# Performance work log

Measured on AMD Instinct MI355X. Metric: run time of the kernel, lower is better.

Reference implementation:

```python
import jax, jax.numpy as jnp
import numpy as np

B, S = 1, 2048
HID, INTER = 4096, 11008
HEADS, HD = 32, 128
GS = 128
EPS = 1e-6
BASE = 10000.0
IMIN, IMAX = -(2**31), 2**31 - 1


def _rope_tables():
    inv_freq = 1.0 / (BASE ** (np.arange(0, HD, 2, dtype=np.float32) / HD))
    t = np.arange(S, dtype=np.float32)
    freqs = np.outer(t, inv_freq)            # [S, HD/2]
    emb = np.concatenate([freqs, freqs], -1)  # [S, HD]
    return jnp.asarray(np.sin(emb), jnp.float32), jnp.asarray(np.cos(emb), jnp.float32)


def setup_inputs() -> dict:
    key = jax.random.key(0)
    ks = iter(jax.random.split(key, 40))
    def qset(in_f, out_f):
        qw = jax.random.randint(next(ks), (in_f // 8, out_f), IMIN, IMAX, dtype=jnp.int32)
        qz = jax.random.randint(next(ks), (in_f // GS, out_f // 8), IMIN, IMAX, dtype=jnp.int32)
        sc = jax.random.uniform(next(ks), (in_f // GS, out_f), dtype=jnp.float32) * 0.01 + 1e-3
        return qw, qz, sc
    dims = {"q": (HID, HID), "k": (HID, HID), "v": (HID, HID), "o": (HID, HID),
            "gate": (HID, INTER), "up": (HID, INTER), "down": (INTER, HID)}
    inp = {}
    for name, (i, o) in dims.items():
        qw, qz, sc = qset(i, o)
        inp["qw_" + name] = qw
        inp["qz_" + name] = qz
        inp["sc_" + name] = sc
    inp["hidden_states"] = jax.random.normal(next(ks), (B, S, HID), dtype=jnp.float32)
    inp["ln1_w"] = jnp.ones((HID,), jnp.float32)
    inp["ln2_w"] = jnp.ones((HID,), jnp.float32)
    sin, cos = _rope_tables()
    inp["sin"] = sin
    inp["cos"] = cos
    # causal additive mask, as stored in ExLlamaBuffer.attn_mask (past_len = 0)
    mask = jnp.where(jnp.tril(jnp.ones((S, S), bool)), 0.0, -1e9).astype(jnp.float32)
    inp["attn_mask"] = mask[None, None]
    return inp


def _dequant(qw, qz, sc):
    # GPTQ int4: qweight [in/8, out] packs 8 rows per int32; qzeros [groups, out/8]
    in_f, out_f = qw.shape[0] * 8, qw.shape[1]
    groups = sc.shape[0]
    sh = jnp.arange(8, dtype=jnp.int32) * 4
    w = ((qw[:, None, :] >> sh[None, :, None]) & 15)
    w = w.reshape(groups, in_f // groups, out_f).astype(jnp.float32)
    z = ((qz[:, :, None] >> sh[None, None, :]) & 15).reshape(groups, out_f).astype(jnp.float32)
    return ((w - (z + 1.0)[:, None, :]) * sc[:, None, :]).reshape(in_f, out_f)


def _rms(x, w):
    v = jnp.mean(x * x, axis=-1, keepdims=True)
    return x * jax.lax.rsqrt(v + EPS) * w


def _rot_half(x):
    x1, x2 = jnp.split(x, 2, axis=-1)
    return jnp.concatenate([-x2, x1], axis=-1)


def reference(qw_q, qz_q, sc_q, qw_k, qz_k, sc_k, qw_v, qz_v, sc_v,
              qw_o, qz_o, sc_o, qw_gate, qz_gate, sc_gate,
              qw_up, qz_up, sc_up, qw_down, qz_down, sc_down,
              hidden_states, ln1_w, ln2_w, sin, cos, attn_mask):
    lin = lambda x, a, b, c: x @ _dequant(a, b, c)
    h = hidden_states
    # attention block
    x = _rms(h, ln1_w)
    q = lin(x, qw_q, qz_q, sc_q).reshape(B, S, HEADS, HD).transpose(0, 2, 1, 3)
    k = lin(x, qw_k, qz_k, sc_k).reshape(B, S, HEADS, HD).transpose(0, 2, 1, 3)
    v = lin(x, qw_v, qz_v, sc_v).reshape(B, S, HEADS, HD).transpose(0, 2, 1, 3)
    c, s = cos[None, None], sin[None, None]  # [1,1,S,HD]
    q = q * c + _rot_half(q) * s
    k = k * c + _rot_half(k) * s
    scores = jnp.einsum('bhqd,bhkd->bhqk', q, k) / np.float32(np.sqrt(HD)) + attn_mask
    p = jax.nn.softmax(scores, axis=-1)
    o = jnp.einsum('bhqk,bhkd->bhqd', p, v).transpose(0, 2, 1, 3).reshape(B, S, HID)
    h = h + lin(o, qw_o, qz_o, sc_o)
    # MLP block
    x = _rms(h, ln2_w)
    y = jax.nn.silu(lin(x, qw_gate, qz_gate, sc_gate)) * lin(x, qw_up, qz_up, sc_up)
    return h + lin(y, qw_down, qz_down, sc_down)
```

## Files before the change

kernel.cpp:

```cpp
#include <hip/hip_runtime.h>
#include <cstdint>
#include <cstddef>

#define S_LEN 2048
#define HID   4096
#define INTER 11008
#define NHEADS 32
#define HD    128

typedef __attribute__((ext_vector_type(4))) float  f32x4;
typedef __attribute__((ext_vector_type(8))) __bf16 bf16x8;
typedef __attribute__((ext_vector_type(8))) short  s16x8;
typedef __attribute__((ext_vector_type(4))) short  s16x4;

__device__ __forceinline__ float bf2f(short s) {
  unsigned u = ((unsigned)(unsigned short)s) << 16;
  return __builtin_bit_cast(float, u);
}
__device__ __forceinline__ short f2bf(float f) {
  unsigned u = __builtin_bit_cast(unsigned, f);
  u += 0x7FFFu + ((u >> 16) & 1u);
  return (short)(u >> 16);
}
__device__ __forceinline__ f32x4 mfma16(s16x8 a, s16x8 b, f32x4 c) {
  return __builtin_amdgcn_mfma_f32_16x16x32_bf16(
      __builtin_bit_cast(bf16x8, a), __builtin_bit_cast(bf16x8, b), c, 0, 0, 0);
}
__device__ __forceinline__ void gload_lds16(const void* g, void* l) {
  __builtin_amdgcn_global_load_lds(
      (const __attribute__((address_space(1))) void*)g,
      (__attribute__((address_space(3))) void*)l, 16, 0, 0);
}

__global__ __launch_bounds__(256) void rmsnorm_kernel(const float* __restrict__ x,
                                                      const float* __restrict__ w,
                                                      short* __restrict__ out) {
  int row = blockIdx.x;
  const float* xr = x + (size_t)row * HID;
  short* orow = out + (size_t)row * HID;
  int tid = threadIdx.x;
  f32x4 v[4];
  float ss = 0.f;
#pragma unroll
  for (int i = 0; i < 4; ++i) {
    v[i] = ((const f32x4*)xr)[i * 256 + tid];
    ss += v[i][0] * v[i][0] + v[i][1] * v[i][1] + v[i][2] * v[i][2] + v[i][3] * v[i][3];
  }
#pragma unroll
  for (int off = 32; off > 0; off >>= 1) ss += __shfl_xor(ss, off);
  __shared__ float psum[4];
  if ((tid & 63) == 0) psum[tid >> 6] = ss;
  __syncthreads();
  float tot = psum[0] + psum[1] + psum[2] + psum[3];
  float r = rsqrtf(tot * (1.0f / (float)HID) + 1e-6f);
#pragma unroll
  for (int i = 0; i < 4; ++i) {
    int base = (i * 256 + tid) * 4;
    s16x4 o;
#pragma unroll
    for (int j = 0; j < 4; ++j) o[j] = f2bf(v[i][j] * r * w[base + j]);
    *(s16x4*)&orow[base] = o;
  }
}

__global__ __launch_bounds__(256) void dequant_kernel(const int* __restrict__ qw,
                                                      const int* __restrict__ qz,
                                                      const float* __restrict__ sc,
                                                      short* __restrict__ wt,
                                                      int N, int noff, int Kext) {
  __shared__ short tile[64 * 72];
  int n0 = blockIdx.x * 64;
  int k0 = blockIdx.y * 64;
  int g = k0 >> 7;
  int qr0 = k0 >> 3;
  int t = threadIdx.x;
#pragma unroll
  for (int i = 0; i < 2; ++i) {
    int idx = t + i * 256;
    int r = idx >> 6;
    int n = idx & 63;
    int gc = noff + n0 + n;
    unsigned q = (unsigned)qw[(size_t)(qr0 + r) * N + gc];
    float s = sc[(size_t)g * N + gc];
    unsigned zq = (unsigned)qz[(size_t)g * (N >> 3) + (gc >> 3)];
    float zs = ((float)((zq >> ((gc & 7) * 4)) & 15u) + 1.0f) * s;
    s16x8 o;
#pragma unroll
    for (int j = 0; j < 8; ++j)
      o[j] = f2bf(fmaf((float)((q >> (4 * j)) & 15u), s, -zs));
    *(s16x8*)&tile[n * 72 + r * 8] = o;
  }
  __syncthreads();
  int n = t >> 2;
#pragma unroll
  for (int i = 0; i < 2; ++i) {
    int c = (t & 3) + i * 4;
    *(s16x8*)&wt[(size_t)(n0 + n) * Kext + k0 + c * 8] = *(const s16x8*)&tile[n * 72 + c * 8];
  }
}

template <int OMODE>
__global__ __launch_bounds__(256) void gemm_kernel(const short* __restrict__ A, int lda,
                                                   const short* __restrict__ BT, int ldb,
                                                   void* __restrict__ Cv, int ldc,
                                                   const float* __restrict__ base,
                                                   int Kext) {
  __shared__ short As[2][128 * 32];
  __shared__ short Bs[2][128 * 32];
  int nwg = gridDim.x * gridDim.y;
  int lid = blockIdx.y * gridDim.x + blockIdx.x;
  int cpx = nwg >> 3;
  int swz = (lid & 7) * cpx + (lid >> 3);
  int bn = swz % gridDim.x, bm = swz / gridDim.x;
  int tid = threadIdx.x;
  int lane = tid & 63, wv = tid >> 6;
  int wr = wv >> 1, wc = wv & 1;
  f32x4 acc[4][4] = {};
  int nk = Kext >> 5;
  int lr = lane >> 2;
  int lc = lane & 3;
  const short* Abase = A + (size_t)(bm * 128) * lda;
  const short* Bbase = BT + (size_t)(bn * 128) * ldb;

  auto stage = [&](int buf, int t) {
    int k0 = t << 5;
#pragma unroll
    for (int i = 0; i < 2; ++i) {
      int r = i * 64 + wv * 16 + lr;
      gload_lds16(Abase + (size_t)r * lda + k0 + lc * 8, &As[buf][i * 2048 + wv * 512]);
      gload_lds16(Bbase + (size_t)r * ldb + k0 + lc * 8, &Bs[buf][i * 2048 + wv * 512]);
    }
  };
  auto compute = [&](int buf) {
    int kc = (lane >> 4) * 8;
    int ra = wr * 64 + (lane & 15);
    int rb = wc * 64 + (lane & 15);
    s16x8 af[4], bfr[4];
#pragma unroll
    for (int m = 0; m < 4; ++m) af[m] = *(const s16x8*)&As[buf][(ra + m * 16) * 32 + kc];
#pragma unroll
    for (int n = 0; n < 4; ++n) bfr[n] = *(const s16x8*)&Bs[buf][(rb + n * 16) * 32 + kc];
#pragma unroll
    for (int m = 0; m < 4; ++m)
#pragma unroll
      for (int n = 0; n < 4; ++n) acc[m][n] = mfma16(af[m], bfr[n], acc[m][n]);
  };

  stage(0, 0);
  __syncthreads();
  for (int t = 0; t < nk; ++t) {
    if (t + 1 < nk) stage((t + 1) & 1, t + 1);
    compute(t & 1);
    __syncthreads();
  }

  int row0 = bm * 128 + wr * 64 + ((lane >> 4) << 2);
  int col0 = bn * 128 + wc * 64 + (lane & 15);
#pragma unroll
  for (int m = 0; m < 4; ++m)
#pragma unroll
    for (int n = 0; n < 4; ++n)
#pragma unroll
      for (int j = 0; j < 4; ++j) {
        size_t idx = (size_t)(row0 + m * 16 + j) * ldc + col0 + n * 16;
        if (OMODE == 0)      ((short*)Cv)[idx] = f2bf(acc[m][n][j]);
        else if (OMODE == 1) ((float*)Cv)[idx] = base[idx] + acc[m][n][j];
        else                 ((float*)Cv)[idx] = ((float*)Cv)[idx] + acc[m][n][j];
      }
}

__global__ __launch_bounds__(128) void rope_kernel(short* __restrict__ q, short* __restrict__ k,
                                                   const float* __restrict__ sp,
                                                   const float* __restrict__ cp) {
  int s = blockIdx.x, h = blockIdx.y;
  short* p = (blockIdx.z ? k : q) + (size_t)s * HID + h * HD;
  int d = threadIdx.x;
  float x = bf2f(p[d]);
  float xp = bf2f(p[d ^ 64]);
  float rot = (d < 64) ? -xp : xp;
  float y = x * cp[s * HD + d] + rot * sp[s * HD + d];
  __syncthreads();
  p[d] = f2bf(y);
}

__global__ __launch_bounds__(256, 2) void attn_kernel(const short* __restrict__ qb,
                                                      const short* __restrict__ kb,
                                                      const short* __restrict__ vb,
                                                      short* __restrict__ ob) {
  int qt = (int)(gridDim.x - 1) - blockIdx.x;
  int h = blockIdx.y;
  int tid = threadIdx.x, lane = tid & 63, wv = tid >> 6;
  __shared__ short Kl[64 * 128];
  __shared__ short Vl[128 * 72];
  __shared__ short Pl[4][32 * 72];
  int q0 = qt * 128 + wv * 32;
  s16x8 qf[2][4];
#pragma unroll
  for (int m = 0; m < 2; ++m)
#pragma unroll
    for (int kf = 0; kf < 4; ++kf) {
      int r = q0 + m * 16 + (lane & 15);
      int d = kf * 32 + (lane >> 4) * 8;
      qf[m][kf] = *(const s16x8*)&qb[(size_t)r * HID + h * HD + d];
    }
  f32x4 o[2][8] = {};
  float mrow[2][4], lrow[2][4];
#pragma unroll
  for (int m = 0; m < 2; ++m)
#pragma unroll
    for (int j = 0; j < 4; ++j) { mrow[m][j] = -1e30f; lrow[m][j] = 0.f; }

  auto load_tile = [&](int kv0, s16x8* kr, s16x8* vr) {
#pragma unroll
    for (int i = 0; i < 4; ++i) {
      int cid = tid + i * 256;
      int kv = cid >> 4, c = cid & 15;
      kr[i] = *(const s16x8*)(kb + (size_t)(kv0 + kv) * HID + h * HD + c * 8);
      vr[i] = *(const s16x8*)(vb + (size_t)(kv0 + kv) * HID + h * HD + c * 8);
    }
  };
  auto store_tile = [&](const s16x8* kr, const s16x8* vr) {
#pragma unroll
    for (int i = 0; i < 4; ++i) {
      int cid = tid + i * 256;
      int kv = cid >> 4, c = cid & 15;
      *(s16x8*)((char*)Kl + kv * 256 + ((c ^ (kv & 7)) * 16)) = kr[i];
      int kvs = kv ^ ((c & 7) << 3);
#pragma unroll
      for (int j = 0; j < 8; ++j) Vl[(c * 8 + j) * 72 + kvs] = vr[i][j];
    }
  };

  const float scale = 0.08838834764831845f;
  int kv_end = qt * 128 + 128;
  s16x8 kra[4], vra[4], krb[4], vrb[4];
  load_tile(0, kra, vra);
  store_tile(kra, vra);
  __syncthreads();
  for (int kv0 = 0; kv0 < kv_end; kv0 += 64) {
    bool more = kv0 + 64 < kv_end;
    if (more) load_tile(kv0 + 64, krb, vrb);

    f32x4 sfr[2][4] = {};
    __builtin_amdgcn_s_setprio(1);
#pragma unroll
    for (int nf = 0; nf < 4; ++nf) {
      s16x8 kfr[4];
      int kvr = nf * 16 + (lane & 15);
#pragma unroll
      for (int kf = 0; kf < 4; ++kf) {
        int cc = (kf * 4 + (lane >> 4)) ^ (kvr & 7);
        kfr[kf] = *(const s16x8*)((const char*)Kl + kvr * 256 + cc * 16);
      }
#pragma unroll
      for (int m = 0; m < 2; ++m)
#pragma unroll
        for (int kf = 0; kf < 4; ++kf) sfr[m][nf] = mfma16(qf[m][kf], kfr[kf], sfr[m][nf]);
    }
    __builtin_amdgcn_s_setprio(0);
#pragma unroll
    for (int m = 0; m < 2; ++m)
#pragma unroll
      for (int j = 0; j < 4; ++j) {
        int qrow = q0 + m * 16 + (lane >> 4) * 4 + j;
        float pm = -1e30f;
#pragma unroll
        for (int nf = 0; nf < 4; ++nf) {
          int kvc = kv0 + nf * 16 + (lane & 15);
          float v = sfr[m][nf][j] * scale;
          v = (kvc <= qrow) ? v : -1e30f;
          sfr[m][nf][j] = v;
          pm = fmaxf(pm, v);
        }
#pragma unroll
        for (int off = 1; off < 16; off <<= 1) pm = fmaxf(pm, __shfl_xor(pm, off));
        float mnew = fmaxf(mrow[m][j], pm);
        float alpha = __expf(mrow[m][j] - mnew);
        mrow[m][j] = mnew;
        float rs = 0.f;
#pragma unroll
        for (int nf = 0; nf < 4; ++nf) {
          float p = __expf(sfr[m][nf][j] - mnew);
          sfr[m][nf][j] = p;
          rs += p;
        }
#pragma unroll
        for (int off = 1; off < 16; off <<= 1) rs += __shfl_xor(rs, off);
        lrow[m][j] = lrow[m][j] * alpha + rs;
#pragma unroll
        for (int nd = 0; nd < 8; ++nd) o[m][nd][j] *= alpha;
      }
#pragma unroll
    for (int m = 0; m < 2; ++m)
#pragma unroll
      for (int nf = 0; nf < 4; ++nf)
#pragma unroll
        for (int j = 0; j < 4; ++j)
          Pl[wv][(m * 16 + (lane >> 4) * 4 + j) * 72 + nf * 16 + (lane & 15)] =
              f2bf(sfr[m][nf][j]);
    s16x8 pa[2][2];
#pragma unroll
    for (int m = 0; m < 2; ++m)
#pragma unroll
      for (int kf = 0; kf < 2; ++kf)
        pa[m][kf] = *(const s16x8*)&Pl[wv][(m * 16 + (lane & 15)) * 72 + kf * 32 + (lane >> 4) * 8];
    __builtin_amdgcn_s_setprio(1);
#pragma unroll
    for (int nd = 0; nd < 8; ++nd) {
      s16x8 vf[2];
      int drow = nd * 16 + (lane & 15);
      int key = ((drow >> 3) & 7) << 3;
#pragma unroll
      for (int kf = 0; kf < 2; ++kf)
        vf[kf] = *(const s16x8*)&Vl[drow * 72 + ((kf * 32 + (lane >> 4) * 8) ^ key)];
#pragma unroll
      for (int m = 0; m < 2; ++m)
#pragma unroll
        for (int kf = 0; kf < 2; ++kf) o[m][nd] = mfma16(pa[m][kf], vf[kf], o[m][nd]);
    }
    __builtin_amdgcn_s_setprio(0);
    __syncthreads();
    if (more) store_tile(krb, vrb);
    __syncthreads();
  }
#pragma unroll
  for (int m = 0; m < 2; ++m)
#pragma unroll
    for (int nd = 0; nd < 8; ++nd)
#pragma unroll
      for (int j = 0; j < 4; ++j) {
        int r = q0 + m * 16 + (lane >> 4) * 4 + j;
        int c = h * HD + nd * 16 + (lane & 15);
        ob[(size_t)r * HID + c] = f2bf(o[m][nd][j] / lrow[m][j]);
      }
}

__global__ __launch_bounds__(256) void silumul_kernel(const short* __restrict__ g,
                                                      const short* __restrict__ u,
                                                      short* __restrict__ y) {
  size_t idx = (size_t)blockIdx.x * 256 + threadIdx.x;
  s16x8 gv = ((const s16x8*)g)[idx];
  s16x8 uv = ((const s16x8*)u)[idx];
  s16x8 yv;
#pragma unroll
  for (int j = 0; j < 8; ++j) {
    float gf = bf2f(gv[j]);
    float uf = bf2f(uv[j]);
    float sl = gf / (1.f + __expf(-gf));
    yv[j] = f2bf(sl * uf);
  }
  ((s16x8*)y)[idx] = yv;
}

extern "C" void kernel_launch(void* const* d_in, const int* in_sizes, int n_in,
                              void* d_out, int out_size, void* d_ws, size_t ws_size,
                              hipStream_t stream) {
  const int* qw[7]; const int* qz[7]; const float* sc[7];
  for (int i = 0; i < 7; ++i) {
    qw[i] = (const int*)d_in[i * 3 + 0];
    qz[i] = (const int*)d_in[i * 3 + 1];
    sc[i] = (const float*)d_in[i * 3 + 2];
  }
  const float* hin  = (const float*)d_in[21];
  const float* ln1  = (const float*)d_in[22];
  const float* ln2  = (const float*)d_in[23];
  const float* sinp = (const float*)d_in[24];
  const float* cosp = (const float*)d_in[25];
  float* out = (float*)d_out;

  char* ws = (char*)d_ws;
  const size_t MB = 1024 * 1024;
  short* XB    = (short*)(ws);
  short* WDQ   = (short*)(ws + 16 * MB);
  short* QB    = (short*)(ws + 48 * MB);
  short* KB    = (short*)(ws + 64 * MB);
  short* VB    = (short*)(ws + 80 * MB);
  short* OB    = (short*)(ws + 96 * MB);
  short* GATEB = (short*)(ws + 48 * MB);
  short* UPB   = (short*)(ws + 91 * MB);

  dim3 blk(256);
  dim3 dq44(64, 64);
  dim3 gm_hid(HID / 128, S_LEN / 128);

  rmsnorm_kernel<<<S_LEN, blk, 0, stream>>>(hin, ln1, XB);
  short* qkv_out[3] = {QB, KB, VB};
  for (int i = 0; i < 3; ++i) {
    dequant_kernel<<<dq44, blk, 0, stream>>>(qw[i], qz[i], sc[i], WDQ, HID, 0, HID);
    gemm_kernel<0><<<gm_hid, blk, 0, stream>>>(XB, HID, WDQ, HID, qkv_out[i], HID, nullptr, HID);
  }
  rope_kernel<<<dim3(S_LEN, NHEADS, 2), dim3(128), 0, stream>>>(QB, KB, sinp, cosp);
  attn_kernel<<<dim3(S_LEN / 128, NHEADS), blk, 0, stream>>>(QB, KB, VB, OB);
  dequant_kernel<<<dq44, blk, 0, stream>>>(qw[3], qz[3], sc[3], WDQ, HID, 0, HID);
  gemm_kernel<1><<<gm_hid, blk, 0, stream>>>(OB, HID, WDQ, HID, out, HID, hin, HID);
  rmsnorm_kernel<<<S_LEN, blk, 0, stream>>>(out, ln2, XB);
  const int noffs[3] = {0, 4096, 8192};
  const int nexts[3] = {4096, 4096, 2816};
  for (int c = 0; c < 3; ++c) {
    dequant_kernel<<<dim3(nexts[c] / 64, 64), blk, 0, stream>>>(qw[4], qz[4], sc[4], WDQ, INTER, noffs[c], HID);
    gemm_kernel<0><<<dim3(nexts[c] / 128, 16), blk, 0, stream>>>(XB, HID, WDQ, HID, GATEB + noffs[c], INTER, nullptr, HID);
  }
  for (int c = 0; c < 3; ++c) {
    dequant_kernel<<<dim3(nexts[c] / 64, 64), blk, 0, stream>>>(qw[5], qz[5], sc[5], WDQ, INTER, noffs[c], HID);
    gemm_kernel<0><<<dim3(nexts[c] / 128, 16), blk, 0, stream>>>(XB, HID, WDQ, HID, UPB + noffs[c], INTER, nullptr, HID);
  }
  silumul_kernel<<<(S_LEN * (size_t)INTER) / 8 / 256, blk, 0, stream>>>(GATEB, UPB, GATEB);
  for (int c = 0; c < 3; ++c) {
    int koff = noffs[c], kx = nexts[c];
    dequant_kernel<<<dim3(64, kx / 64), blk, 0, stream>>>(
        qw[6] + (size_t)(koff >> 3) * HID, qz[6] + (size_t)(koff >> 7) * (HID / 8),
        sc[6] + (size_t)(koff >> 7) * HID, WDQ, HID, 0, kx);
    gemm_kernel<2><<<gm_hid, blk, 0, stream>>>(GATEB + koff, INTER, WDQ, kx, out, HID, nullptr, kx);
  }
}
```

Baseline: 1.582 ms.

## Overlap next weight dequant with current GEMM in a combined kernel launch

Merges dequant and GEMM into one kernel whose grid splits into GEMM blocks and dequant blocks. Each launch runs a GEMM on one ping-pong weight buffer while dequantizing the next weight into the other buffer, which removes serialization between dequant and GEMM launches. The SiLU-multiply is fused into the up-projection epilogue, dropping the separate elementwise pass and the UP buffer. Attention launch bounds change to one block per SM, and Q is staged in the output buffer. Buffer aliasing and chunk offsets are intricate, so a small indexing error could corrupt results.

```diff
diff --git a/kernel.cpp b/kernel.cpp
--- a/kernel.cpp
+++ b/kernel.cpp
@@ -63,110 +63,115 @@
   }
 }
 
-__global__ __launch_bounds__(256) void dequant_kernel(const int* __restrict__ qw,
-                                                      const int* __restrict__ qz,
-                                                      const float* __restrict__ sc,
-                                                      short* __restrict__ wt,
-                                                      int N, int noff, int Kext) {
-  __shared__ short tile[64 * 72];
-  int n0 = blockIdx.x * 64;
-  int k0 = blockIdx.y * 64;
-  int g = k0 >> 7;
-  int qr0 = k0 >> 3;
-  int t = threadIdx.x;
-#pragma unroll
-  for (int i = 0; i < 2; ++i) {
-    int idx = t + i * 256;
-    int r = idx >> 6;
-    int n = idx & 63;
-    int gc = noff + n0 + n;
-    unsigned q = (unsigned)qw[(size_t)(qr0 + r) * N + gc];
-    float s = sc[(size_t)g * N + gc];
-    unsigned zq = (unsigned)qz[(size_t)g * (N >> 3) + (gc >> 3)];
-    float zs = ((float)((zq >> ((gc & 7) * 4)) & 15u) + 1.0f) * s;
-    s16x8 o;
-#pragma unroll
-    for (int j = 0; j < 8; ++j)
-      o[j] = f2bf(fmaf((float)((q >> (4 * j)) & 15u), s, -zs));
-    *(s16x8*)&tile[n * 72 + r * 8] = o;
+template <int OMODE>
+__global__ __launch_bounds__(256) void paired_kernel(
+    const short* __restrict__ A, int lda,
+    const short* __restrict__ BT, int ldb,
+    void* __restrict__ Cv, int ldc,
+    const float* __restrict__ base, int Kext,
+    int gnx, int gny,
+    const int* __restrict__ qw, const int* __restrict__ qz,
+    const float* __restrict__ sc, short* __restrict__ wt,
+    int N, int noff, int dnx, int dqld) {
+  __shared__ short sm[4 * 4096];
+  int bid = blockIdx.x;
+  int gtot = gnx * gny;
+  int tid = threadIdx.x;
+  if (bid < gtot) {
+    int cpx = gtot >> 3;
+    int swz = (bid & 7) * cpx + (bid >> 3);
+    int bn = swz % gnx, bm = swz / gnx;
+    int lane = tid & 63, wv = tid >> 6;
+    int wr = wv >> 1, wc = wv & 1;
+    f32x4 acc[4][4] = {};
+    int nk = Kext >> 5;
+    int lr = lane >> 2, lc = lane & 3;
+    const short* Abase = A + (size_t)(bm * 128) * lda;
+    const short* Bbase = BT + (size_t)(bn * 128) * ldb;
+    short* As0 = sm;
+    short* Bs0 = sm + 8192;
+
+    auto stage = [&](int buf, int t) {
+      int k0 = t << 5;
+#pragma unroll
+      for (int i = 0; i < 2; ++i) {
+        int r = i * 64 + wv * 16 + lr;
+        gload_lds16(Abase + (size_t)r * lda + k0 + lc * 8, As0 + buf * 4096 + i * 2048 + wv * 512);
+        gload_lds16(Bbase + (size_t)r * ldb + k0 + lc * 8, Bs0 + buf * 4096 + i * 2048 + wv * 512);
+      }
+    };
+    auto compute = [&](int buf) {
+      int kc = (lane >> 4) * 8;
+      int ra = wr * 64 + (lane & 15);
+      int rb = wc * 64 + (lane & 15);
+      s16x8 af[4], bfr[4];
+#pragma unroll
+      for (int m = 0; m < 4; ++m) af[m] = *(const s16x8*)&As0[buf * 4096 + (ra + m * 16) * 32 + kc];
+#pragma unroll
+      for (int n = 0; n < 4; ++n) bfr[n] = *(const s16x8*)&Bs0[buf * 4096 + (rb + n * 16) * 32 + kc];
+#pragma unroll
+      for (int m = 0; m < 4; ++m)
+#pragma unroll
+        for (int n = 0; n < 4; ++n) acc[m][n] = mfma16(af[m], bfr[n], acc[m][n]);
+    };
+
+    stage(0, 0);
+    __syncthreads();
+    for (int t = 0; t < nk; ++t) {
+      if (t + 1 < nk) stage((t + 1) & 1, t + 1);
+      compute(t & 1);
+      __syncthreads();
+    }
+
+    int row0 = bm * 128 + wr * 64 + ((lane >> 4) << 2);
+    int col0 = bn * 128 + wc * 64 + (lane & 15);
+#pragma unroll
+    for (int m = 0; m < 4; ++m)
+#pragma unroll
+      for (int n = 0; n < 4; ++n)
+#pragma unroll
+        for (int j = 0; j < 4; ++j) {
+          size_t idx = (size_t)(row0 + m * 16 + j) * ldc + col0 + n * 16;
+          if (OMODE == 0)      ((short*)Cv)[idx] = f2bf(acc[m][n][j]);
+          else if (OMODE == 1) ((float*)Cv)[idx] = base[idx] + acc[m][n][j];
+          else if (OMODE == 2) ((float*)Cv)[idx] = ((float*)Cv)[idx] + acc[m][n][j];
+          else {
+            short* C = (short*)Cv;
+            float g = bf2f(C[idx]);
+            float sl = g / (1.f + __expf(-g));
+            C[idx] = f2bf(sl * acc[m][n][j]);
+          }
+        }
+  } else {
+    int id = bid - gtot;
+    int n0 = (id % dnx) * 64;
+    int k0 = (id / dnx) * 64;
+    int g = k0 >> 7;
+    int qr0 = k0 >> 3;
+#pragma unroll
+    for (int i = 0; i < 2; ++i) {
+      int idx = tid + i * 256;
+      int r = idx >> 6;
+      int n = idx & 63;
+      int gc = noff + n0 + n;
+      unsigned q = (unsigned)qw[(size_t)(qr0 + r) * N + gc];
+      float s = sc[(size_t)g * N + gc];
+      unsigned zq = (unsigned)qz[(size_t)g * (N >> 3) + (gc >> 3)];
+      float zs = ((float)((zq >> ((gc & 7) * 4)) & 15u) + 1.0f) * s;
+      s16x8 o;
+#pragma unroll
+      for (int j = 0; j < 8; ++j)
+        o[j] = f2bf(fmaf((float)((q >> (4 * j)) & 15u), s, -zs));
+      *(s16x8*)&sm[n * 72 + r * 8] = o;
+    }
+    __syncthreads();
+    int n = tid >> 2;
+#pragma unroll
+    for (int i = 0; i < 2; ++i) {
+      int c = (tid & 3) + i * 4;
+      *(s16x8*)&wt[(size_t)(n0 + n) * dqld + k0 + c * 8] = *(const s16x8*)&sm[n * 72 + c * 8];
+    }
   }
-  __syncthreads();
-  int n = t >> 2;
-#pragma unroll
-  for (int i = 0; i < 2; ++i) {
-    int c = (t & 3) + i * 4;
-    *(s16x8*)&wt[(size_t)(n0 + n) * Kext + k0 + c * 8] = *(const s16x8*)&tile[n * 72 + c * 8];
-  }
-}
-
-template <int OMODE>
-__global__ __launch_bounds__(256) void gemm_kernel(const short* __restrict__ A, int lda,
-                                                   const short* __restrict__ BT, int ldb,
-                                                   void* __restrict__ Cv, int ldc,
-                                                   const float* __restrict__ base,
-                                                   int Kext) {
-  __shared__ short As[2][128 * 32];
-  __shared__ short Bs[2][128 * 32];
-  int nwg = gridDim.x * gridDim.y;
-  int lid = blockIdx.y * gridDim.x + blockIdx.x;
-  int cpx = nwg >> 3;
-  int swz = (lid & 7) * cpx + (lid >> 3);
-  int bn = swz % gridDim.x, bm = swz / gridDim.x;
-  int tid = threadIdx.x;
-  int lane = tid & 63, wv = tid >> 6;
-  int wr = wv >> 1, wc = wv & 1;
-  f32x4 acc[4][4] = {};
-  int nk = Kext >> 5;
-  int lr = lane >> 2;
-  int lc = lane & 3;
-  const short* Abase = A + (size_t)(bm * 128) * lda;
-  const short* Bbase = BT + (size_t)(bn * 128) * ldb;
-
-  auto stage = [&](int buf, int t) {
-    int k0 = t << 5;
-#pragma unroll
-    for (int i = 0; i < 2; ++i) {
-      int r = i * 64 + wv * 16 + lr;
-      gload_lds16(Abase + (size_t)r * lda + k0 + lc * 8, &As[buf][i * 2048 + wv * 512]);
-      gload_lds16(Bbase + (size_t)r * ldb + k0 + lc * 8, &Bs[buf][i * 2048 + wv * 512]);
-    }
-  };
-  auto compute = [&](int buf) {
-    int kc = (lane >> 4) * 8;
-    int ra = wr * 64 + (lane & 15);
-    int rb = wc * 64 + (lane & 15);
-    s16x8 af[4], bfr[4];
-#pragma unroll
-    for (int m = 0; m < 4; ++m) af[m] = *(const s16x8*)&As[buf][(ra + m * 16) * 32 + kc];
-#pragma unroll
-    for (int n = 0; n < 4; ++n) bfr[n] = *(const s16x8*)&Bs[buf][(rb + n * 16) * 32 + kc];
-#pragma unroll
-    for (int m = 0; m < 4; ++m)
-#pragma unroll
-      for (int n = 0; n < 4; ++n) acc[m][n] = mfma16(af[m], bfr[n], acc[m][n]);
-  };
-
-  stage(0, 0);
-  __syncthreads();
-  for (int t = 0; t < nk; ++t) {
-    if (t + 1 < nk) stage((t + 1) & 1, t + 1);
-    compute(t & 1);
-    __syncthreads();
-  }
-
-  int row0 = bm * 128 + wr * 64 + ((lane >> 4) << 2);
-  int col0 = bn * 128 + wc * 64 + (lane & 15);
-#pragma unroll
-  for (int m = 0; m < 4; ++m)
-#pragma unroll
-    for (int n = 0; n < 4; ++n)
-#pragma unroll
-      for (int j = 0; j < 4; ++j) {
-        size_t idx = (size_t)(row0 + m * 16 + j) * ldc + col0 + n * 16;
-        if (OMODE == 0)      ((short*)Cv)[idx] = f2bf(acc[m][n][j]);
-        else if (OMODE == 1) ((float*)Cv)[idx] = base[idx] + acc[m][n][j];
-        else                 ((float*)Cv)[idx] = ((float*)Cv)[idx] + acc[m][n][j];
-      }
 }
 
 __global__ __launch_bounds__(128) void rope_kernel(short* __restrict__ q, short* __restrict__ k,
@@ -183,7 +188,7 @@
   p[d] = f2bf(y);
 }
 
-__global__ __launch_bounds__(256, 2) void attn_kernel(const short* __restrict__ qb,
+__global__ __launch_bounds__(256, 1) void attn_kernel(const short* __restrict__ qb,
                                                       const short* __restrict__ kb,
                                                       const short* __restrict__ vb,
                                                       short* __restrict__ ob) {
@@ -333,23 +338,6 @@
         int c = h * HD + nd * 16 + (lane & 15);
         ob[(size_t)r * HID + c] = f2bf(o[m][nd][j] / lrow[m][j]);
       }
-}
-
-__global__ __launch_bounds__(256) void silumul_kernel(const short* __restrict__ g,
-                                                      const short* __restrict__ u,
-                                                      short* __restrict__ y) {
-  size_t idx = (size_t)blockIdx.x * 256 + threadIdx.x;
-  s16x8 gv = ((const s16x8*)g)[idx];
-  s16x8 uv = ((const s16x8*)u)[idx];
-  s16x8 yv;
-#pragma unroll
-  for (int j = 0; j < 8; ++j) {
-    float gf = bf2f(gv[j]);
-    float uf = bf2f(uv[j]);
-    float sl = gf / (1.f + __expf(-gf));
-    yv[j] = f2bf(sl * uf);
-  }
-  ((s16x8*)y)[idx] = yv;
 }
 
 extern "C" void kernel_launch(void* const* d_in, const int* in_sizes, int n_in,
@@ -371,45 +359,57 @@
   char* ws = (char*)d_ws;
   const size_t MB = 1024 * 1024;
   short* XB    = (short*)(ws);
-  short* WDQ   = (short*)(ws + 16 * MB);
-  short* QB    = (short*)(ws + 48 * MB);
-  short* KB    = (short*)(ws + 64 * MB);
-  short* VB    = (short*)(ws + 80 * MB);
-  short* OB    = (short*)(ws + 96 * MB);
-  short* GATEB = (short*)(ws + 48 * MB);
-  short* UPB   = (short*)(ws + 91 * MB);
+  short* WA    = (short*)(ws + 16 * MB);
+  short* WB    = (short*)(ws + 48 * MB);
+  short* KB    = (short*)(ws + 80 * MB);
+  short* VB    = (short*)(ws + 96 * MB);
+  short* OB    = (short*)(ws + 112 * MB);
+  short* GATEB = (short*)(ws + 80 * MB);
+  short* QBd   = (short*)d_out;
 
   dim3 blk(256);
-  dim3 dq44(64, 64);
-  dim3 gm_hid(HID / 128, S_LEN / 128);
-
-  rmsnorm_kernel<<<S_LEN, blk, 0, stream>>>(hin, ln1, XB);
-  short* qkv_out[3] = {QB, KB, VB};
-  for (int i = 0; i < 3; ++i) {
-    dequant_kernel<<<dq44, blk, 0, stream>>>(qw[i], qz[i], sc[i], WDQ, HID, 0, HID);
-    gemm_kernel<0><<<gm_hid, blk, 0, stream>>>(XB, HID, WDQ, HID, qkv_out[i], HID, nullptr, HID);
-  }
-  rope_kernel<<<dim3(S_LEN, NHEADS, 2), dim3(128), 0, stream>>>(QB, KB, sinp, cosp);
-  attn_kernel<<<dim3(S_LEN / 128, NHEADS), blk, 0, stream>>>(QB, KB, VB, OB);
-  dequant_kernel<<<dq44, blk, 0, stream>>>(qw[3], qz[3], sc[3], WDQ, HID, 0, HID);
-  gemm_kernel<1><<<gm_hid, blk, 0, stream>>>(OB, HID, WDQ, HID, out, HID, hin, HID);
-  rmsnorm_kernel<<<S_LEN, blk, 0, stream>>>(out, ln2, XB);
   const int noffs[3] = {0, 4096, 8192};
   const int nexts[3] = {4096, 4096, 2816};
-  for (int c = 0; c < 3; ++c) {
-    dequant_kernel<<<dim3(nexts[c] / 64, 64), blk, 0, stream>>>(qw[4], qz[4], sc[4], WDQ, INTER, noffs[c], HID);
-    gemm_kernel<0><<<dim3(nexts[c] / 128, 16), blk, 0, stream>>>(XB, HID, WDQ, HID, GATEB + noffs[c], INTER, nullptr, HID);
-  }
-  for (int c = 0; c < 3; ++c) {
-    dequant_kernel<<<dim3(nexts[c] / 64, 64), blk, 0, stream>>>(qw[5], qz[5], sc[5], WDQ, INTER, noffs[c], HID);
-    gemm_kernel<0><<<dim3(nexts[c] / 128, 16), blk, 0, stream>>>(XB, HID, WDQ, HID, UPB + noffs[c], INTER, nullptr, HID);
-  }
-  silumul_kernel<<<(S_LEN * (size_t)INTER) / 8 / 256, blk, 0, stream>>>(GATEB, UPB, GATEB);
-  for (int c = 0; c < 3; ++c) {
-    int koff = noffs[c], kx = nexts[c];
-    dequant_kernel<<<dim3(64, kx / 64), blk, 0, stream>>>(
-        qw[6] + (size_t)(koff >> 3) * HID, qz[6] + (size_t)(koff >> 7) * (HID / 8),
-        sc[6] + (size_t)(koff >> 7) * HID, WDQ, HID, 0, kx);
-    gemm_kernel<2><<<gm_hid, blk, 0, stream>>>(GATEB + koff, INTER, WDQ, kx, out, HID, nullptr, kx);
-  }
-}
+
+  rmsnorm_kernel<<<S_LEN, blk, 0, stream>>>(hin, ln1, XB);
+  paired_kernel<0><<<4096, blk, 0, stream>>>(nullptr, 0, nullptr, 0, nullptr, 0, nullptr, 0,
+                                             0, 0, qw[0], qz[0], sc[0], WA, HID, 0, 64, HID);
+  paired_kernel<0><<<512 + 4096, blk, 0, stream>>>(XB, HID, WA, HID, QBd, HID, nullptr, HID,
+                                                   32, 16, qw[1], qz[1], sc[1], WB, HID, 0, 64, HID);
+  paired_kernel<0><<<512 + 4096, blk, 0, stream>>>(XB, HID, WB, HID, KB, HID, nullptr, HID,
+                                                   32, 16, qw[2], qz[2], sc[2], WA, HID, 0, 64, HID);
+  paired_kernel<0><<<512 + 4096, blk, 0, stream>>>(XB, HID, WA, HID, VB, HID, nullptr, HID,
+                                                   32, 16, qw[3], qz[3], sc[3], WB, HID, 0, 64, HID);
+  rope_kernel<<<dim3(S_LEN, NHEADS, 2), dim3(128), 0, stream>>>(QBd, KB, sinp, cosp);
+  attn_kernel<<<dim3(S_LEN / 128, NHEADS), blk, 0, stream>>>(QBd, KB, VB, OB);
+  paired_kernel<1><<<512 + 4096, blk, 0, stream>>>(OB, HID, WB, HID, out, HID, hin, HID,
+                                                   32, 16, qw[4], qz[4], sc[4], WA, INTER, 0, 64, HID);
+  rmsnorm_kernel<<<S_LEN, blk, 0, stream>>>(out, ln2, XB);
+
+  paired_kernel<0><<<512 + 4096, blk, 0, stream>>>(XB, HID, WA, HID, GATEB + 0, INTER, nullptr, HID,
+                                                   32, 16, qw[5], qz[5], sc[5], WB, INTER, 0, 64, HID);
+  paired_kernel<3><<<512 + 4096, blk, 0, stream>>>(XB, HID, WB, HID, GATEB + 0, INTER, nullptr, HID,
+                                                   32, 16, qw[4], qz[4], sc[4], WA, INTER, 4096, 64, HID);
+  paired_kernel<0><<<512 + 4096, blk, 0, stream>>>(XB, HID, WA, HID, GATEB + 4096, INTER, nullptr, HID,
+                                                   32, 16, qw[5], qz[5], sc[5], WB, INTER, 4096, 64, HID);
+  paired_kernel<3><<<512 + 2816, blk, 0, stream>>>(XB, HID, WB, HID, GATEB + 4096, INTER, nullptr, HID,
+                                                   32, 16, qw[4], qz[4], sc[4], WA, INTER, 8192, 44, HID);
+  paired_kernel<0><<<352 + 2816, blk, 0, stream>>>(XB, HID, WA, HID, GATEB + 8192, INTER, nullptr, HID,
+                                                   22, 16, qw[5], qz[5], sc[5], WB, INTER, 8192, 44, HID);
+  paired_kernel<3><<<352 + 4096, blk, 0, stream>>>(XB, HID, WB, HID, GATEB + 8192, INTER, nullptr, HID,
+                                                   22, 16, qw[6], qz[6], sc[6], WA, HID, 0, 64, 4096);
+  paired_kernel<2><<<512 + 4096, blk, 0, stream>>>(GATEB + 0, INTER, WA, 4096, out, HID, nullptr, 4096,
+                                                   32, 16,
+                                                   qw[6] + (size_t)(4096 >> 3) * HID,
+                                                   qz[6] + (size_t)(4096 >> 7) * (HID / 8),
+                                                   sc[6] + (size_t)(4096 >> 7) * HID,
+                                                   WB, HID, 0, 64, 4096);
+  paired_kernel<2><<<512 + 2816, blk, 0, stream>>>(GATEB + 4096, INTER, WB, 4096, out, HID, nullptr, 4096,
+                                                   32, 16,
+                                                   qw[6] + (size_t)(8192 >> 3) * HID,
+                                                   qz[6] + (size_t)(8192 >> 7) * (HID / 8),
+                                                   sc[6] + (size_t)(8192 >> 7) * HID,
+                                                   WA, HID, 0, 64, 2816);
+  paired_kernel<2><<<512, blk, 0, stream>>>(GATEB + 8192, INTER, WA, 2816, out, HID, nullptr, 2816,
+                                            32, 16, nullptr, nullptr, nullptr, nullptr, HID, 0, 1, HID);
+}
```

Result: faster. 1.461 ms (-7.7%).
